# Kernel optimization log

Hardware: AMD Instinct MI355X
Metric: run time of the kernel (lower is better)

The kernel has to match this reference:

```python
import jax, jax.numpy as jnp
import numpy as np

N = 100000       # num nodes
E = 1600000      # num edges (avg degree 16)
IN_DIM = 256
EMB_DIM = 128
K = 2            # nlayers: number of propagation steps


def setup_inputs() -> dict:
    key = jax.random.key(0)
    k1, k2, k3, k4, k5 = jax.random.split(key, 5)
    x = jax.random.normal(k1, (N, IN_DIM), dtype=jnp.float32)
    # glorot-initialized linear weight + zero bias
    scale = jnp.sqrt(6.0 / (IN_DIM + EMB_DIM))
    W = jax.random.uniform(k2, (IN_DIM, EMB_DIM), minval=-scale, maxval=scale, dtype=jnp.float32)
    b = jnp.zeros((EMB_DIM,), dtype=jnp.float32)
    edge_src = jax.random.randint(k3, (E,), 0, N, dtype=jnp.int32)
    edge_dst = jax.random.randint(k4, (E,), 0, N, dtype=jnp.int32)
    # normalized-adjacency-like edge weights (positive, ~1/deg scale)
    edge_w = jax.random.uniform(k5, (E,), dtype=jnp.float32) * (1.0 / 16.0)
    return {"x": x, "W": W, "b": b, "edge_src": edge_src, "edge_dst": edge_dst, "edge_w": edge_w}


def reference(x, W, b, edge_src, edge_dst, edge_w):
    # dropout is identity in eval mode; linear + relu
    h = jax.nn.relu(x @ W + b)  # [N, EMB_DIM]
    # k-step sparse propagation: h <- g @ h, g given as COO edge list
    for _ in range(K):
        msg = h[edge_src] * edge_w[:, None]                     # [E, EMB_DIM]
        h = jax.ops.segment_sum(msg, edge_dst, num_segments=N)  # [N, EMB_DIM]
    return h
```

## Files before the change

### kernel.cpp

```cpp
#include <hip/hip_runtime.h>

#define IN_DIM 256
#define EMB 128
#define BKT_SHIFT 9
#define BKT_NODES 512

typedef __attribute__((ext_vector_type(8))) short short8;
typedef __attribute__((ext_vector_type(4))) float f32x4;

__device__ __forceinline__ unsigned short bf16rtne(float f) {
    unsigned int u = __float_as_uint(f);
    return (unsigned short)((u + 0x7fffu + ((u >> 16) & 1u)) >> 16);
}

__device__ __forceinline__ unsigned int packbf2(float lo, float hi) {
    return ((unsigned int)bf16rtne(hi) << 16) | (unsigned int)bf16rtne(lo);
}

__device__ __forceinline__ short8 pack8(float4 f0, float4 f1) {
    union { uint4 u; short8 s; } U;
    asm("v_cvt_pk_bf16_f32 %0, %1, %2" : "=v"(U.u.x) : "v"(f0.x), "v"(f0.y));
    asm("v_cvt_pk_bf16_f32 %0, %1, %2" : "=v"(U.u.y) : "v"(f0.z), "v"(f0.w));
    asm("v_cvt_pk_bf16_f32 %0, %1, %2" : "=v"(U.u.z) : "v"(f1.x), "v"(f1.y));
    asm("v_cvt_pk_bf16_f32 %0, %1, %2" : "=v"(U.u.w) : "v"(f1.z), "v"(f1.w));
    return U.s;
}


__global__ __launch_bounds__(256) void bucket_hist(const int* __restrict__ dst,
                                                   int* __restrict__ ghist, int E) {
    __shared__ int h[256];
    int t = threadIdx.x;
    h[t] = 0;
    __syncthreads();
    int e0 = blockIdx.x * 1024;
    int e1 = min(E, e0 + 1024);
    for (int i = e0 + t; i < e1; i += 256) atomicAdd(&h[dst[i] >> BKT_SHIFT], 1);
    __syncthreads();
    if (h[t]) atomicAdd(&ghist[t], h[t]);
}

__global__ __launch_bounds__(256) void bucket_scan(const int* __restrict__ ghist,
                                                   int* __restrict__ bucket_off,
                                                   int* __restrict__ gcursor,
                                                   int* __restrict__ row_ptr,
                                                   int NB, int N, int E) {
    __shared__ int s[256];
    int t = threadIdx.x;
    int v = (t < NB) ? ghist[t] : 0;
    s[t] = v;
    __syncthreads();
    for (int off = 1; off < 256; off <<= 1) {
        int u = (t >= off) ? s[t - off] : 0;
        __syncthreads();
        s[t] += u;
        __syncthreads();
    }
    int excl = s[t] - v;
    if (t < NB) {
        bucket_off[t] = excl;
        gcursor[t] = excl;
    }
    if (t == 0) {
        bucket_off[NB] = E;
        row_ptr[N] = E;
    }
}


__global__ __launch_bounds__(512) void bin_scatter(const int* __restrict__ src,
                                                   const int* __restrict__ dst,
                                                   const float* __restrict__ w,
                                                   int* __restrict__ gcursor,
                                                   int2* __restrict__ binned, int E) {
    __shared__ int h[256];
    __shared__ int cur[256];
    int t = threadIdx.x;
    if (t < 256) h[t] = 0;
    __syncthreads();
    int e0 = blockIdx.x * 4096;
    int e1 = min(E, e0 + 4096);
    for (int i = e0 + t; i < e1; i += 512) atomicAdd(&h[dst[i] >> BKT_SHIFT], 1);
    __syncthreads();
    if (t < 256) cur[t] = h[t] ? atomicAdd(&gcursor[t], h[t]) : 0;
    __syncthreads();
    for (int i = e0 + t; i < e1; i += 512) {
        int d = dst[i];
        int b = d >> BKT_SHIFT;
        int ld = d & (BKT_NODES - 1);
        int pos = atomicAdd(&cur[b], 1);
        int2 r;
        r.x = src[i] | (ld << 17);
        r.y = __float_as_int(w[i]);
        binned[pos] = r;
    }
}


__global__ __launch_bounds__(1024) void bucket_sort(const int2* __restrict__ binned,
                                                    const int* __restrict__ bucket_off,
                                                    int2* __restrict__ sorted,
                                                    int* __restrict__ row_ptr, int N) {
    __shared__ int cnt[BKT_NODES];
    __shared__ int cur[BKT_NODES];
    __shared__ int scn[BKT_NODES];
    int t = threadIdx.x;
    int b = blockIdx.x;
    int node0 = b << BKT_SHIFT;
    int nn = min(BKT_NODES, N - node0);
    int beg = bucket_off[b];
    int endb = bucket_off[b + 1];
    if (t < BKT_NODES) cnt[t] = 0;
    __syncthreads();
    for (int i = beg + t; i < endb; i += 1024) {
        int ld = ((unsigned int)binned[i].x) >> 17;
        atomicAdd(&cnt[ld], 1);
    }
    __syncthreads();
    int v = 0;
    if (t < BKT_NODES) {
        v = cnt[t];
        scn[t] = v;
    }
    __syncthreads();
    for (int off = 1; off < BKT_NODES; off <<= 1) {
        int u = 0;
        if (t < BKT_NODES && t >= off) u = scn[t - off];
        __syncthreads();
        if (t < BKT_NODES) scn[t] += u;
        __syncthreads();
    }
    if (t < BKT_NODES) {
        int ep = beg + scn[t] - v;
        cur[t] = ep;
        if (t < nn) row_ptr[node0 + t] = ep;
    }
    __syncthreads();
    for (int i = beg + t; i < endb; i += 1024) {
        int2 r = binned[i];
        int ld = ((unsigned int)r.x) >> 17;
        int pos = atomicAdd(&cur[ld], 1);
        r.x &= 0x1FFFF;
        sorted[pos] = r;
    }
}


__global__ __launch_bounds__(256) void wt_cast(const float* __restrict__ W,
                                               unsigned short* __restrict__ wtg) {
    int i = blockIdx.x * 256 + threadIdx.x;
    int c = i & 127;
    int k = i >> 7;
    wtg[c * 256 + k] = bf16rtne(W[(size_t)k * 128 + c]);
}


__global__ __launch_bounds__(256) void gemm_mfma(const float* __restrict__ x,
                                                 const unsigned short* __restrict__ wtg,
                                                 const float* __restrict__ bias,
                                                 unsigned short* __restrict__ hbf, int N) {
    __shared__ unsigned short xs[64][64];
    __shared__ unsigned short wsh[128][64];
    int tid = threadIdx.x;
    int row0 = blockIdx.x * 64;
    int wv = tid >> 6;
    int lane = tid & 63;
    int lr = lane & 15;
    int lg = lane >> 4;
    int wr = wv * 16;

    f32x4 acc[8];
#pragma unroll
    for (int n = 0; n < 8; ++n) acc[n] = (f32x4){0.f, 0.f, 0.f, 0.f};

    int xrow = tid >> 2;
    int xk0 = (tid & 3) * 16;
    bool xvalid = (row0 + xrow) < N;
    const float* xsrc = x + (size_t)(row0 + xrow) * IN_DIM + xk0;
    int wcol = tid >> 1;
    int wk0 = (tid & 1) * 32;
    const unsigned short* wsrc = wtg + (size_t)wcol * IN_DIM + wk0;
    const float4 zf4 = make_float4(0.f, 0.f, 0.f, 0.f);

    int arow = wr + lr;
    int asw = (arow & 7) << 3;

    for (int kb = 0; kb < IN_DIM; kb += 64) {
        float4 f0 = xvalid ? ((const float4*)(xsrc + kb))[0] : zf4;
        float4 f1 = xvalid ? ((const float4*)(xsrc + kb))[1] : zf4;
        float4 f2 = xvalid ? ((const float4*)(xsrc + kb))[2] : zf4;
        float4 f3 = xvalid ? ((const float4*)(xsrc + kb))[3] : zf4;
#pragma unroll
        for (int j = 0; j < 4; ++j) {
            uint4 v = ((const uint4*)(wsrc + kb))[j];
            int ko = (wk0 + j * 8) ^ ((wcol & 7) << 3);
            *(uint4*)&wsh[wcol][ko] = v;
        }
        short8 p0 = pack8(f0, f1);
        short8 p1 = pack8(f2, f3);
        int xsw = (xrow & 7) << 3;
        *(short8*)&xs[xrow][xk0 ^ xsw] = p0;
        *(short8*)&xs[xrow][(xk0 + 8) ^ xsw] = p1;
        __syncthreads();

        short8 a0 = *(const short8*)&xs[arow][(lg * 8) ^ asw];
        short8 a1 = *(const short8*)&xs[arow][(32 + lg * 8) ^ asw];
#pragma unroll
        for (int n = 0; n < 8; ++n) {
            int c = n * 16 + lr;
            int sw = (c & 7) << 3;
            short8 b0 = *(const short8*)&wsh[c][(lg * 8) ^ sw];
            short8 b1 = *(const short8*)&wsh[c][(32 + lg * 8) ^ sw];
            acc[n] = __builtin_amdgcn_mfma_f32_16x16x32_bf16(a0, b0, acc[n], 0, 0, 0);
            acc[n] = __builtin_amdgcn_mfma_f32_16x16x32_bf16(a1, b1, acc[n], 0, 0, 0);
        }
        __syncthreads();
    }

#pragma unroll
    for (int n = 0; n < 8; ++n) {
        int c = n * 16 + lr;
        float bv = bias[c];
#pragma unroll
        for (int j = 0; j < 4; ++j) {
            int r = row0 + wr + lg * 4 + j;
            if (r < N) {
                float v = fmaxf(acc[n][j] + bv, 0.f);
                hbf[(size_t)r * EMB + c] = bf16rtne(v);
            }
        }
    }
}


template <int OUTBF>
__global__ __launch_bounds__(256) void prop_g(const unsigned int* __restrict__ hin,
                                              void* __restrict__ hout,
                                              const int* __restrict__ rp,
                                              const int2* __restrict__ rec, int N) {
    int wvid = threadIdx.x >> 6;
    int lane = threadIdx.x & 63;
    int node = blockIdx.x * 4 + wvid;
    if (node >= N) return;
    int beg = __builtin_amdgcn_readfirstlane(rp[node]);
    int end = __builtin_amdgcn_readfirstlane(rp[node + 1]);
    float ax = 0.f, ay = 0.f;
    for (int c0 = beg; c0 < end; c0 += 64) {
        int cnt = end - c0;
        if (cnt > 64) cnt = 64;
        int li = lane < cnt ? lane : 0;
        int2 r = rec[c0 + li];
        for (int jb = 0; jb < cnt; jb += 8) {
            int ssrc[8];
            float sw[8];
#pragma unroll
            for (int k = 0; k < 8; ++k) {
                int jj = jb + k;
                int jc = jj < cnt ? jj : 0;
                ssrc[k] = __builtin_amdgcn_readlane(r.x, jc);
                float wv = __uint_as_float((unsigned int)__builtin_amdgcn_readlane(r.y, jc));
                sw[k] = (jj < cnt) ? wv : 0.f;
            }
            unsigned int g[8];
#pragma unroll
            for (int k = 0; k < 8; ++k) g[k] = hin[(size_t)ssrc[k] * 64 + lane];
#pragma unroll
            for (int k = 0; k < 8; ++k) {
                ax = fmaf(sw[k], __uint_as_float(g[k] << 16), ax);
                ay = fmaf(sw[k], __uint_as_float(g[k] & 0xffff0000u), ay);
            }
        }
    }
    if (OUTBF) {
        ((unsigned int*)hout)[(size_t)node * 64 + lane] = packbf2(ax, ay);
    } else {
        float2 o;
        o.x = ax;
        o.y = ay;
        ((float2*)hout)[(size_t)node * 64 + lane] = o;
    }
}


extern "C" void kernel_launch(void* const* d_in, const int* in_sizes, int n_in,
                              void* d_out, int out_size, void* d_ws, size_t ws_size,
                              hipStream_t stream) {
    const float* x = (const float*)d_in[0];
    const float* W = (const float*)d_in[1];
    const float* b = (const float*)d_in[2];
    const int* esrc = (const int*)d_in[3];
    const int* edst = (const int*)d_in[4];
    const float* ew = (const float*)d_in[5];
    int N = in_sizes[0] / IN_DIM;
    int E = in_sizes[3];
    int NB = (N + BKT_NODES - 1) >> BKT_SHIFT;

    char* p = (char*)d_ws;
    auto alloc = [&](size_t bytes) -> void* {
        void* r = (void*)p;
        p += (bytes + 255) & ~(size_t)255;
        return r;
    };
    unsigned short* hbf = (unsigned short*)alloc((size_t)N * EMB * 2);
    unsigned short* h1bf = (unsigned short*)alloc((size_t)N * EMB * 2);
    unsigned short* wtg = (unsigned short*)alloc((size_t)IN_DIM * EMB * 2);
    int* ghist = (int*)alloc(256 * 4);
    int* gcursor = (int*)alloc(256 * 4);
    int* bucket_off = (int*)alloc((size_t)(NB + 1) * 4);
    int* row_ptr = (int*)alloc((size_t)(N + 1) * 4);
    int2* binned = (int2*)alloc((size_t)E * 8);
    int2* sorted = (int2*)alloc((size_t)E * 8);

    hipMemsetAsync(ghist, 0, 256 * 4, stream);
    wt_cast<<<(IN_DIM * EMB) / 256, 256, 0, stream>>>(W, wtg);
    bucket_hist<<<(E + 1023) / 1024, 256, 0, stream>>>(edst, ghist, E);
    bucket_scan<<<1, 256, 0, stream>>>(ghist, bucket_off, gcursor, row_ptr, NB, N, E);
    bin_scatter<<<(E + 4095) / 4096, 512, 0, stream>>>(esrc, edst, ew, gcursor, binned, E);
    bucket_sort<<<NB, 1024, 0, stream>>>(binned, bucket_off, sorted, row_ptr, N);

    gemm_mfma<<<(N + 63) / 64, 256, 0, stream>>>(x, wtg, b, hbf, N);
    prop_g<1><<<(N + 3) / 4, 256, 0, stream>>>((const unsigned int*)hbf, h1bf, row_ptr, sorted, N);
    prop_g<0><<<(N + 3) / 4, 256, 0, stream>>>((const unsigned int*)h1bf, d_out, row_ptr, sorted, N);
}
```

Baseline: 273.6 us.

## Load GEMM A operands directly to registers and stage full W tile once

The GEMM kernel no longer stages x through shared memory in four K-chunks. Each lane now loads its row's x values straight into registers in MFMA operand layout and converts them to bf16 in place. The whole 128x256 bf16 weight matrix is loaded into LDS once, followed by a single barrier. This removes the per-chunk barriers and the LDS round trip for x, at the cost of 64KB of LDS per block and more registers, which may lower occupancy.

```diff
diff --git a/kernel.cpp b/kernel.cpp
--- a/kernel.cpp
+++ b/kernel.cpp
@@ -159,62 +159,53 @@
                                                  const unsigned short* __restrict__ wtg,
                                                  const float* __restrict__ bias,
                                                  unsigned short* __restrict__ hbf, int N) {
-    __shared__ unsigned short xs[64][64];
-    __shared__ unsigned short wsh[128][64];
+    __shared__ unsigned short wsh[128][256];
     int tid = threadIdx.x;
-    int row0 = blockIdx.x * 64;
     int wv = tid >> 6;
     int lane = tid & 63;
     int lr = lane & 15;
     int lg = lane >> 4;
-    int wr = wv * 16;
+    int row0 = blockIdx.x * 64;
+    int row = row0 + wv * 16 + lr;
+    bool valid = row < N;
+    const float4* xr = (const float4*)(x + (size_t)row * IN_DIM);
+    const float4 zf4 = make_float4(0.f, 0.f, 0.f, 0.f);
+
+    float4 xf[16];
+#pragma unroll
+    for (int kk = 0; kk < 8; ++kk) {
+#pragma unroll
+        for (int j = 0; j < 2; ++j)
+            xf[kk * 2 + j] = valid ? xr[kk * 8 + lg * 2 + j] : zf4;
+    }
+
+#pragma unroll
+    for (int j = 0; j < 16; ++j) {
+        int ci = tid + 256 * j;
+        int c = ci >> 5;
+        int k0 = (ci & 31) * 8;
+        uint4 v = *(const uint4*)(wtg + c * 256 + k0);
+        *(uint4*)&wsh[c][k0 ^ ((c & 7) << 3)] = v;
+    }
+
+    short8 a[8];
+#pragma unroll
+    for (int kk = 0; kk < 8; ++kk) a[kk] = pack8(xf[kk * 2], xf[kk * 2 + 1]);
 
     f32x4 acc[8];
 #pragma unroll
     for (int n = 0; n < 8; ++n) acc[n] = (f32x4){0.f, 0.f, 0.f, 0.f};
 
-    int xrow = tid >> 2;
-    int xk0 = (tid & 3) * 16;
-    bool xvalid = (row0 + xrow) < N;
-    const float* xsrc = x + (size_t)(row0 + xrow) * IN_DIM + xk0;
-    int wcol = tid >> 1;
-    int wk0 = (tid & 1) * 32;
-    const unsigned short* wsrc = wtg + (size_t)wcol * IN_DIM + wk0;
-    const float4 zf4 = make_float4(0.f, 0.f, 0.f, 0.f);
-
-    int arow = wr + lr;
-    int asw = (arow & 7) << 3;
-
-    for (int kb = 0; kb < IN_DIM; kb += 64) {
-        float4 f0 = xvalid ? ((const float4*)(xsrc + kb))[0] : zf4;
-        float4 f1 = xvalid ? ((const float4*)(xsrc + kb))[1] : zf4;
-        float4 f2 = xvalid ? ((const float4*)(xsrc + kb))[2] : zf4;
-        float4 f3 = xvalid ? ((const float4*)(xsrc + kb))[3] : zf4;
-#pragma unroll
-        for (int j = 0; j < 4; ++j) {
-            uint4 v = ((const uint4*)(wsrc + kb))[j];
-            int ko = (wk0 + j * 8) ^ ((wcol & 7) << 3);
-            *(uint4*)&wsh[wcol][ko] = v;
-        }
-        short8 p0 = pack8(f0, f1);
-        short8 p1 = pack8(f2, f3);
-        int xsw = (xrow & 7) << 3;
-        *(short8*)&xs[xrow][xk0 ^ xsw] = p0;
-        *(short8*)&xs[xrow][(xk0 + 8) ^ xsw] = p1;
-        __syncthreads();
-
-        short8 a0 = *(const short8*)&xs[arow][(lg * 8) ^ asw];
-        short8 a1 = *(const short8*)&xs[arow][(32 + lg * 8) ^ asw];
+    __syncthreads();
+
+#pragma unroll
+    for (int kk = 0; kk < 8; ++kk) {
 #pragma unroll
         for (int n = 0; n < 8; ++n) {
             int c = n * 16 + lr;
-            int sw = (c & 7) << 3;
-            short8 b0 = *(const short8*)&wsh[c][(lg * 8) ^ sw];
-            short8 b1 = *(const short8*)&wsh[c][(32 + lg * 8) ^ sw];
-            acc[n] = __builtin_amdgcn_mfma_f32_16x16x32_bf16(a0, b0, acc[n], 0, 0, 0);
-            acc[n] = __builtin_amdgcn_mfma_f32_16x16x32_bf16(a1, b1, acc[n], 0, 0, 0);
+            short8 b = *(const short8*)&wsh[c][(kk * 32 + lg * 8) ^ ((c & 7) << 3)];
+            acc[n] = __builtin_amdgcn_mfma_f32_16x16x32_bf16(a[kk], b, acc[n], 0, 0, 0);
         }
-        __syncthreads();
     }
 
 #pragma unroll
@@ -223,7 +214,7 @@
         float bv = bias[c];
 #pragma unroll
         for (int j = 0; j < 4; ++j) {
-            int r = row0 + wr + lg * 4 + j;
+            int r = row0 + wv * 16 + lg * 4 + j;
             if (r < N) {
                 float v = fmaxf(acc[n][j] + bv, 0.f);
                 hbf[(size_t)r * EMB + c] = bf16rtne(v);
```

After: 278.0 us. About the same (+1.6%).
